# Kernel optimization log

Measured on AMD Instinct MI355X. Metric: run time of the kernel, lower is better.

The kernel has to match this reference:

```python
import jax, jax.numpy as jnp
import numpy as np

IN_C, OUT_C, EDGE_C = 128, 64, 1
N_NODES, N_EDGES = 50000, 800000


def setup_inputs() -> dict:
    key = jax.random.key(0)
    ks = jax.random.split(key, 12)
    d = OUT_C
    # xavier-uniform-ish scales
    def xav(k, shape):
        lim = float(np.sqrt(6.0 / (shape[0] + shape[1])))
        return jax.random.uniform(k, shape, jnp.float32, -lim, lim)
    return {
        "feat_src": jax.random.normal(ks[0], (N_NODES, IN_C), jnp.float32),
        "feat_dst": jax.random.normal(ks[1], (N_NODES, IN_C), jnp.float32),
        "edge_weight": jax.random.uniform(ks[2], (N_EDGES, EDGE_C), jnp.float32),
        "src_idx": jax.random.randint(ks[3], (N_EDGES,), 0, N_NODES),
        "dst_idx": jnp.sort(jax.random.randint(ks[4], (N_EDGES,), 0, N_NODES)),
        "weight_n": xav(ks[5], (IN_C, d)),
        "weight_e": xav(ks[6], (EDGE_C, d)),
        "query": xav(ks[7], (d, d)),
        "key_w": xav(ks[8], (d, d)),
        "att_w": xav(ks[9], (3 * d, 1)),
        "att_b": jnp.zeros((1,), jnp.float32),
        "out_w": xav(ks[10], (2 * d, d)),
        "out_b": jnp.zeros((d,), jnp.float32),
    }


def reference(feat_src, feat_dst, edge_weight, src_idx, dst_idx,
              weight_n, weight_e, query, key_w, att_w, att_b, out_w, out_b):
    d = query.shape[0]
    n_dst = feat_dst.shape[0]
    h_src = feat_src @ weight_n                      # [N_src, d]
    h_dst = feat_dst @ weight_n                      # [N_dst, d]
    edge_emb = edge_weight @ weight_e                # [E, d]
    q_e = (h_dst @ query)[dst_idx]                   # [E, d] gather
    k_e = (h_src @ key_w)[src_idx]                   # [E, d] gather
    # linear_att(concat([q, k, e])) without materializing the concat
    logits = (q_e @ att_w[:d] + k_e @ att_w[d:2 * d]
              + edge_emb @ att_w[2 * d:] + att_b)    # [E, 1]
    logits = jax.nn.leaky_relu(logits, 0.2)
    # segment softmax over destination nodes
    m = jax.ops.segment_max(logits, dst_idx, num_segments=n_dst)   # [N_dst, 1]
    ex = jnp.exp(logits - m[dst_idx])
    s = jax.ops.segment_sum(ex, dst_idx, num_segments=n_dst)       # [N_dst, 1]
    alpha = ex / (s[dst_idx] + 1e-16)                # [E, 1]
    msg = alpha * h_src[src_idx]                     # [E, d]
    agg = jax.ops.segment_sum(msg, dst_idx, num_segments=n_dst)    # [N_dst, d]
    # linear_out(concat([h_dst, agg]))
    out = h_dst @ out_w[:d] + agg @ out_w[d:] + out_b
    return out
```

## Files before the change

kernel.cpp:

```cpp
#include <hip/hip_runtime.h>
#include <hip/hip_bf16.h>

typedef short short8 __attribute__((ext_vector_type(8)));
typedef float float4v __attribute__((ext_vector_type(4)));
typedef unsigned short ushort4v __attribute__((ext_vector_type(4)));

static __device__ __forceinline__ short f2b(float f) {
    union { __hip_bfloat16 b; short s; } v;
    v.b = __float2bfloat16(f);
    return v.s;
}
static __device__ __forceinline__ float b2f(unsigned short u) {
    union { float f; unsigned v; } x;
    x.v = ((unsigned)u) << 16;
    return x.f;
}

__global__ void __launch_bounds__(256) setup_kernel(
    const float* __restrict__ query, const float* __restrict__ key_w,
    const float* __restrict__ weight_e, const float* __restrict__ att_w,
    const float* __restrict__ Wn, const float* __restrict__ out_w,
    const int* __restrict__ dst_idx,
    unsigned short* __restrict__ BTs, unsigned short* __restrict__ BTd,
    float* __restrict__ Wk, float* __restrict__ Wq, float* __restrict__ escale,
    int* __restrict__ row_ptr, int n_nodes, int n_edges) {
    int b = blockIdx.x, t = threadIdx.x;
    if (b < 64) {
        int idx = b * 256 + t;
        int mat = idx >> 13;
        int rem = idx & 8191;
        int n = rem >> 7, k = rem & 127;
        float s = 0.f;
        for (int m = 0; m < 64; ++m)
            s += Wn[k * 64 + m] * out_w[(mat ? m : 64 + m) * 64 + n];
        (mat ? BTd : BTs)[n * 128 + k] = (unsigned short)f2b(s);
    } else if (b == 64) {
        __shared__ float kq[128];
        __shared__ float ep[64];
        if (t < 64) {
            float s = 0.f;
            for (int j = 0; j < 64; ++j) s += key_w[t * 64 + j] * att_w[64 + j];
            kq[t] = s;
        } else if (t < 128) {
            int i = t - 64;
            float s = 0.f;
            for (int j = 0; j < 64; ++j) s += query[i * 64 + j] * att_w[j];
            kq[64 + i] = s;
        } else if (t < 192) {
            int j = t - 128;
            ep[j] = weight_e[j] * att_w[128 + j];
        }
        __syncthreads();
        if (t < 128) {
            float s = 0.f;
            for (int k = 0; k < 64; ++k) s += Wn[t * 64 + k] * kq[k];
            Wk[t] = s;
        } else {
            int i = t - 128;
            float s = 0.f;
            for (int k = 0; k < 64; ++k) s += Wn[i * 64 + k] * kq[64 + k];
            Wq[i] = s;
        }
        if (t == 0) {
            float s = 0.f;
            for (int j = 0; j < 64; ++j) s += ep[j];
            escale[0] = s;
        }
    } else {
        int idx = (b - 65) * 256 + t;
        if (idx > n_nodes) return;
        int lo = 0, hi = n_edges;
        while (lo < hi) {
            int mid = (lo + hi) >> 1;
            if (dst_idx[mid] < idx) lo = mid + 1; else hi = mid;
        }
        row_ptr[idx] = lo;
    }
}

__global__ void __launch_bounds__(256) gemm_kernel(
    const float* __restrict__ feat_src, const float* __restrict__ feat_dst,
    const unsigned short* __restrict__ BTs, const unsigned short* __restrict__ BTd,
    const float* __restrict__ Wk, const float* __restrict__ Wq,
    unsigned short* __restrict__ hw2, float* __restrict__ out,
    const float* __restrict__ out_b, float* __restrict__ kscore,
    float* __restrict__ qscore, int n_nodes, int nb) {
    int t = threadIdx.x;
    bool isSrc = (int)blockIdx.x < nb;
    int bs = isSrc ? blockIdx.x : blockIdx.x - nb;
    int wave = t >> 6, lane = t & 63;
    int m15 = lane & 15, quad = lane >> 4;
    const unsigned short* BT = isSrc ? BTs : BTd;
    const float* A = isSrc ? feat_src : feat_dst;
    const float* w = isSrc ? Wk : Wq;

    short8 bf[4][4];
#pragma unroll
    for (int kk = 0; kk < 4; ++kk)
#pragma unroll
        for (int nt = 0; nt < 4; ++nt)
            bf[kk][nt] = *(const short8*)(BT + (nt * 16 + m15) * 128 + kk * 32 + quad * 8);
    float4v w0[4], w1[4];
#pragma unroll
    for (int kk = 0; kk < 4; ++kk) {
        w0[kk] = *(const float4v*)(w + kk * 32 + quad * 8);
        w1[kk] = *(const float4v*)(w + kk * 32 + quad * 8 + 4);
    }

#pragma unroll
    for (int tt = 0; tt < 2; ++tt) {
        int rb = ((bs * 4 + wave) * 2 + tt) * 16;
        if (rb >= n_nodes) continue;
        const float* Arow = A + (size_t)(rb + m15) * 128 + quad * 8;

        float4v acc[4] = {};
        float sk = 0.f;
#pragma unroll
        for (int kk = 0; kk < 4; ++kk) {
            float4v a0 = *(const float4v*)(Arow + kk * 32);
            float4v a1 = *(const float4v*)(Arow + kk * 32 + 4);
#pragma unroll
            for (int j = 0; j < 4; ++j) sk += a0[j] * w0[kk][j] + a1[j] * w1[kk][j];
            short8 a;
#pragma unroll
            for (int j = 0; j < 4; ++j) { a[j] = f2b(a0[j]); a[4 + j] = f2b(a1[j]); }
#pragma unroll
            for (int nt = 0; nt < 4; ++nt)
                acc[nt] = __builtin_amdgcn_mfma_f32_16x16x32_bf16(a, bf[kk][nt], acc[nt], 0, 0, 0);
        }
#pragma unroll
        for (int nt = 0; nt < 4; ++nt) {
            int col = nt * 16 + m15;
            float bv = isSrc ? 0.f : out_b[col];
#pragma unroll
            for (int r = 0; r < 4; ++r) {
                int row = rb + quad * 4 + r;
                if (isSrc) hw2[(size_t)row * 64 + col] = (unsigned short)f2b(acc[nt][r]);
                else       out[(size_t)row * 64 + col] = acc[nt][r] + bv;
            }
        }
        sk += __shfl_xor(sk, 16);
        sk += __shfl_xor(sk, 32);
        if (quad == 0) {
            if (isSrc) kscore[rb + m15] = sk;
            else       qscore[rb + m15] = sk;
        }
    }
}

__global__ void __launch_bounds__(256) agg_kernel(
    const int* __restrict__ src_idx, const float* __restrict__ edge_w,
    const unsigned short* __restrict__ hw2, const float* __restrict__ kscore,
    const float* __restrict__ qscore, const float* __restrict__ escale_p,
    const float* __restrict__ att_b, const int* __restrict__ row_ptr,
    float* __restrict__ out, int n_nodes) {
    int wid = (int)((blockIdx.x * blockDim.x + threadIdx.x) >> 6);
    int lane = threadIdx.x & 63;
    int n0 = wid * 2;
    if (n0 >= n_nodes) return;
    int nCnt = (n0 + 1 < n_nodes) ? 2 : 1;
    int rp0 = row_ptr[n0];
    int rp1 = row_ptr[n0 + 1];
    int rp2 = (nCnt == 2) ? row_ptr[n0 + 2] : rp1;
    int total = rp2 - rp0;
    if (total == 0) return;
    float escale = escale_p[0];
    float bias = att_b[0];
    int eslot = lane >> 4, cg = lane & 15;

    if (total <= 64) {
        int m = rp1 - rp0;
        int s0 = 0; float w = 0.f;
        if (lane < total) {
            s0 = src_idx[rp0 + lane];
            float lg = qscore[n0 + (lane >= m ? 1 : 0)] + kscore[s0]
                     + edge_w[rp0 + lane] * escale + bias;
            lg = (lg > 0.f) ? lg : 0.2f * lg;
            w = __expf(fminf(lg, 80.f));
        }
        float pre = w;
#pragma unroll
        for (int off = 1; off < 64; off <<= 1) {
            float tv = __shfl_up(pre, off);
            if (lane >= off) pre += tv;
        }
        float sumAll = __shfl(pre, 63);
        float sum0 = (m > 0) ? __shfl(pre, m - 1) : 0.f;
        float sum1 = sumAll - sum0;
        float mySum = (lane >= m) ? sum1 : sum0;
        float alpha0 = w * (1.f / (mySum + 1e-16f));

        for (int j = 0; j < nCnt; ++j) {
            int sl = j ? m : 0;
            int deg = j ? (total - m) : m;
            if (deg == 0) continue;
            float ac0 = 0.f, ac1 = 0.f, ac2 = 0.f, ac3 = 0.f;
            for (int b = 0; b < deg; b += 4) {
                int eo = b + eslot;
                int idx = (eo < deg) ? (sl + eo) : sl;
                float alpha = __shfl(alpha0, idx);
                int s = __shfl(s0, idx);
                if (eo >= deg) alpha = 0.f;
                ushort4v h = *(const ushort4v*)(hw2 + (size_t)s * 64 + cg * 4);
                ac0 += alpha * b2f(h[0]);
                ac1 += alpha * b2f(h[1]);
                ac2 += alpha * b2f(h[2]);
                ac3 += alpha * b2f(h[3]);
            }
            ac0 += __shfl_xor(ac0, 16); ac0 += __shfl_xor(ac0, 32);
            ac1 += __shfl_xor(ac1, 16); ac1 += __shfl_xor(ac1, 32);
            ac2 += __shfl_xor(ac2, 16); ac2 += __shfl_xor(ac2, 32);
            ac3 += __shfl_xor(ac3, 16); ac3 += __shfl_xor(ac3, 32);
            if (lane < 16) {
                float* op = out + (size_t)(n0 + j) * 64 + lane * 4;
                float4v bb = *(const float4v*)op;
                bb[0] += ac0; bb[1] += ac1; bb[2] += ac2; bb[3] += ac3;
                *(float4v*)op = bb;
            }
        }
    } else {
        for (int j = 0; j < nCnt; ++j) {
            int start = (j == 0) ? rp0 : rp1;
            int deg = ((j == 0) ? rp1 : rp2) - start;
            if (deg == 0) continue;
            float qs = qscore[n0 + j];
            float ac0 = 0.f, ac1 = 0.f, ac2 = 0.f, ac3 = 0.f;
            if (deg <= 64) {
                int s0 = 0; float lg0 = -1e30f;
                if (lane < deg) {
                    s0 = src_idx[start + lane];
                    float lg = qs + kscore[s0] + edge_w[start + lane] * escale + bias;
                    lg0 = (lg > 0.f) ? lg : 0.2f * lg;
                }
                float mx = lg0;
#pragma unroll
                for (int off = 32; off; off >>= 1) mx = fmaxf(mx, __shfl_xor(mx, off));
                float a0 = __expf(lg0 - mx);
                float sm = a0;
#pragma unroll
                for (int off = 32; off; off >>= 1) sm += __shfl_xor(sm, off);
                float alpha0 = a0 * (1.f / (sm + 1e-16f));
                for (int b = 0; b < deg; b += 4) {
                    int eo = b + eslot;
                    int idx = (eo < deg) ? eo : 0;
                    float alpha = __shfl(alpha0, idx);
                    int s = __shfl(s0, idx);
                    if (eo >= deg) alpha = 0.f;
                    ushort4v h = *(const ushort4v*)(hw2 + (size_t)s * 64 + cg * 4);
                    ac0 += alpha * b2f(h[0]);
                    ac1 += alpha * b2f(h[1]);
                    ac2 += alpha * b2f(h[2]);
                    ac3 += alpha * b2f(h[3]);
                }
            } else {
                float mx = -1e30f, sm = 0.f;
                for (int eo = lane; eo < deg; eo += 64) {
                    int s = src_idx[start + eo];
                    float lg = qs + kscore[s] + edge_w[start + eo] * escale + bias;
                    lg = (lg > 0.f) ? lg : 0.2f * lg;
                    float nm = fmaxf(mx, lg);
                    sm = sm * __expf(mx - nm) + __expf(lg - nm);
                    mx = nm;
                }
                for (int off = 32; off; off >>= 1) {
                    float m2 = __shfl_xor(mx, off);
                    float s2 = __shfl_xor(sm, off);
                    float nm = fmaxf(mx, m2);
                    sm = sm * __expf(mx - nm) + s2 * __expf(m2 - nm);
                    mx = nm;
                }
                float inv = 1.f / (sm + 1e-16f);
                for (int b = 0; b < deg; b += 4) {
                    int eo = b + eslot;
                    bool valid = eo < deg;
                    int e = start + (valid ? eo : 0);
                    int s = src_idx[e];
                    float lg = qs + kscore[s] + edge_w[e] * escale + bias;
                    lg = (lg > 0.f) ? lg : 0.2f * lg;
                    float alpha = valid ? __expf(lg - mx) * inv : 0.f;
                    ushort4v h = *(const ushort4v*)(hw2 + (size_t)s * 64 + cg * 4);
                    ac0 += alpha * b2f(h[0]);
                    ac1 += alpha * b2f(h[1]);
                    ac2 += alpha * b2f(h[2]);
                    ac3 += alpha * b2f(h[3]);
                }
            }
            ac0 += __shfl_xor(ac0, 16); ac0 += __shfl_xor(ac0, 32);
            ac1 += __shfl_xor(ac1, 16); ac1 += __shfl_xor(ac1, 32);
            ac2 += __shfl_xor(ac2, 16); ac2 += __shfl_xor(ac2, 32);
            ac3 += __shfl_xor(ac3, 16); ac3 += __shfl_xor(ac3, 32);
            if (lane < 16) {
                float* op = out + (size_t)(n0 + j) * 64 + lane * 4;
                float4v bb = *(const float4v*)op;
                bb[0] += ac0; bb[1] += ac1; bb[2] += ac2; bb[3] += ac3;
                *(float4v*)op = bb;
            }
        }
    }
}

extern "C" void kernel_launch(void* const* d_in, const int* in_sizes, int n_in,
                              void* d_out, int out_size, void* d_ws, size_t ws_size,
                              hipStream_t stream) {
    const float* feat_src = (const float*)d_in[0];
    const float* feat_dst = (const float*)d_in[1];
    const float* edge_w   = (const float*)d_in[2];
    const int*   src_idx  = (const int*)d_in[3];
    const int*   dst_idx  = (const int*)d_in[4];
    const float* weight_n = (const float*)d_in[5];
    const float* weight_e = (const float*)d_in[6];
    const float* query    = (const float*)d_in[7];
    const float* key_w    = (const float*)d_in[8];
    const float* att_w    = (const float*)d_in[9];
    const float* att_b    = (const float*)d_in[10];
    const float* out_w    = (const float*)d_in[11];
    const float* out_b    = (const float*)d_in[12];
    float* out = (float*)d_out;

    int n_nodes = in_sizes[0] / 128;
    int n_edges = in_sizes[3];

    char* p = (char*)d_ws;
    unsigned short* hw2 = (unsigned short*)p;  p += (size_t)n_nodes * 64 * 2;
    float* kscore = (float*)p;  p += (size_t)n_nodes * 4;
    float* qscore = (float*)p;  p += (size_t)n_nodes * 4;
    unsigned short* BTs = (unsigned short*)p;  p += 64 * 128 * 2;
    unsigned short* BTd = (unsigned short*)p;  p += 64 * 128 * 2;
    float* Wk     = (float*)p;  p += 128 * 4;
    float* Wq     = (float*)p;  p += 128 * 4;
    float* escale = (float*)p;  p += 64;
    int*  row_ptr = (int*)p;

    int rp_blocks = (n_nodes + 1 + 255) / 256;
    hipLaunchKernelGGL(setup_kernel, dim3(65 + rp_blocks), dim3(256), 0, stream,
                       query, key_w, weight_e, att_w, weight_n, out_w, dst_idx,
                       BTs, BTd, Wk, Wq, escale, row_ptr, n_nodes, n_edges);

    int nb = (n_nodes + 127) / 128;
    hipLaunchKernelGGL(gemm_kernel, dim3(2 * nb), dim3(256), 0, stream,
                       feat_src, feat_dst, BTs, BTd, Wk, Wq,
                       hw2, out, out_b, kscore, qscore, n_nodes, nb);

    int n_waves = (n_nodes + 1) / 2;
    hipLaunchKernelGGL(agg_kernel, dim3((n_waves + 3) / 4), dim3(256), 0, stream,
                       src_idx, edge_w, hw2, kscore, qscore,
                       escale, att_b, row_ptr, out, n_nodes);
}
```

Before: 163.8 us.

## Stage GEMM weight tile in padded LDS and issue A loads before barrier

The node-projection GEMM kernel now loads the bf16 weight matrix once per block into padded shared memory instead of holding 16 short8 fragments per lane in registers. Each wave handles one 16-row tile instead of two, so the grid doubles, and each lane issues its A-row loads before the LDS fill and barrier so the two overlap. The aim is lower register pressure, higher occupancy and more memory parallelism, at the cost of LDS reads per MFMA and a block-wide sync.

```diff
diff --git a/kernel.cpp b/kernel.cpp
--- a/kernel.cpp
+++ b/kernel.cpp
@@ -85,66 +85,71 @@
     unsigned short* __restrict__ hw2, float* __restrict__ out,
     const float* __restrict__ out_b, float* __restrict__ kscore,
     float* __restrict__ qscore, int n_nodes, int nb) {
+    __shared__ __align__(16) unsigned short BT[64 * 136];
     int t = threadIdx.x;
     bool isSrc = (int)blockIdx.x < nb;
     int bs = isSrc ? blockIdx.x : blockIdx.x - nb;
     int wave = t >> 6, lane = t & 63;
     int m15 = lane & 15, quad = lane >> 4;
-    const unsigned short* BT = isSrc ? BTs : BTd;
+
+    int rb = bs * 64 + wave * 16;
+    bool valid = rb < n_nodes;
+
     const float* A = isSrc ? feat_src : feat_dst;
+    float4v a0[4], a1[4];
+    if (valid) {
+        const float* Arow = A + (size_t)(rb + m15) * 128 + quad * 8;
+#pragma unroll
+        for (int kk = 0; kk < 4; ++kk) {
+            a0[kk] = *(const float4v*)(Arow + kk * 32);
+            a1[kk] = *(const float4v*)(Arow + kk * 32 + 4);
+        }
+    }
+
+    const unsigned short* BTg = isSrc ? BTs : BTd;
+#pragma unroll
+    for (int i = 0; i < 4; ++i) {
+        int j = i * 256 + t;
+        int n = j >> 4, k8 = (j & 15) * 8;
+        *(short8*)(&BT[n * 136 + k8]) = *(const short8*)(BTg + n * 128 + k8);
+    }
+    __syncthreads();
+    if (!valid) return;
+
     const float* w = isSrc ? Wk : Wq;
-
-    short8 bf[4][4];
-#pragma unroll
-    for (int kk = 0; kk < 4; ++kk)
-#pragma unroll
-        for (int nt = 0; nt < 4; ++nt)
-            bf[kk][nt] = *(const short8*)(BT + (nt * 16 + m15) * 128 + kk * 32 + quad * 8);
-    float4v w0[4], w1[4];
+    float4v acc[4] = {};
+    float sk = 0.f;
 #pragma unroll
     for (int kk = 0; kk < 4; ++kk) {
-        w0[kk] = *(const float4v*)(w + kk * 32 + quad * 8);
-        w1[kk] = *(const float4v*)(w + kk * 32 + quad * 8 + 4);
-    }
-
-#pragma unroll
-    for (int tt = 0; tt < 2; ++tt) {
-        int rb = ((bs * 4 + wave) * 2 + tt) * 16;
-        if (rb >= n_nodes) continue;
-        const float* Arow = A + (size_t)(rb + m15) * 128 + quad * 8;
-
-        float4v acc[4] = {};
-        float sk = 0.f;
-#pragma unroll
-        for (int kk = 0; kk < 4; ++kk) {
-            float4v a0 = *(const float4v*)(Arow + kk * 32);
-            float4v a1 = *(const float4v*)(Arow + kk * 32 + 4);
-#pragma unroll
-            for (int j = 0; j < 4; ++j) sk += a0[j] * w0[kk][j] + a1[j] * w1[kk][j];
-            short8 a;
-#pragma unroll
-            for (int j = 0; j < 4; ++j) { a[j] = f2b(a0[j]); a[4 + j] = f2b(a1[j]); }
-#pragma unroll
-            for (int nt = 0; nt < 4; ++nt)
-                acc[nt] = __builtin_amdgcn_mfma_f32_16x16x32_bf16(a, bf[kk][nt], acc[nt], 0, 0, 0);
-        }
+        float4v w0 = *(const float4v*)(w + kk * 32 + quad * 8);
+        float4v w1 = *(const float4v*)(w + kk * 32 + quad * 8 + 4);
+#pragma unroll
+        for (int j = 0; j < 4; ++j) sk += a0[kk][j] * w0[j] + a1[kk][j] * w1[j];
+        short8 a;
+#pragma unroll
+        for (int j = 0; j < 4; ++j) { a[j] = f2b(a0[kk][j]); a[4 + j] = f2b(a1[kk][j]); }
 #pragma unroll
         for (int nt = 0; nt < 4; ++nt) {
-            int col = nt * 16 + m15;
-            float bv = isSrc ? 0.f : out_b[col];
-#pragma unroll
-            for (int r = 0; r < 4; ++r) {
-                int row = rb + quad * 4 + r;
-                if (isSrc) hw2[(size_t)row * 64 + col] = (unsigned short)f2b(acc[nt][r]);
-                else       out[(size_t)row * 64 + col] = acc[nt][r] + bv;
-            }
-        }
-        sk += __shfl_xor(sk, 16);
-        sk += __shfl_xor(sk, 32);
-        if (quad == 0) {
-            if (isSrc) kscore[rb + m15] = sk;
-            else       qscore[rb + m15] = sk;
-        }
+            short8 bb = *(const short8*)(&BT[(nt * 16 + m15) * 136 + kk * 32 + quad * 8]);
+            acc[nt] = __builtin_amdgcn_mfma_f32_16x16x32_bf16(a, bb, acc[nt], 0, 0, 0);
+        }
+    }
+#pragma unroll
+    for (int nt = 0; nt < 4; ++nt) {
+        int col = nt * 16 + m15;
+        float bv = isSrc ? 0.f : out_b[col];
+#pragma unroll
+        for (int r = 0; r < 4; ++r) {
+            int row = rb + quad * 4 + r;
+            if (isSrc) hw2[(size_t)row * 64 + col] = (unsigned short)f2b(acc[nt][r]);
+            else       out[(size_t)row * 64 + col] = acc[nt][r] + bv;
+        }
+    }
+    sk += __shfl_xor(sk, 16);
+    sk += __shfl_xor(sk, 32);
+    if (quad == 0) {
+        if (isSrc) kscore[rb + m15] = sk;
+        else       qscore[rb + m15] = sk;
     }
 }
 
@@ -336,7 +341,7 @@
                        query, key_w, weight_e, att_w, weight_n, out_w, dst_idx,
                        BTs, BTd, Wk, Wq, escale, row_ptr, n_nodes, n_edges);
 
-    int nb = (n_nodes + 127) / 128;
+    int nb = (n_nodes + 63) / 64;
     hipLaunchKernelGGL(gemm_kernel, dim3(2 * nb), dim3(256), 0, stream,
                        feat_src, feat_dst, BTs, BTd, Wk, Wq,
                        hw2, out, out_b, kscore, qscore, n_nodes, nb);
```

Measured after the change: 154.3 us, median of 2. -5.8%, faster.
